# Kernel optimization log

Hardware: AMD Instinct MI355X
Metric: run time of the kernel (lower is better)

## Reference

```python
import jax, jax.numpy as jnp
import numpy as np

RADIUS = 0.4
NSAMPLE = 32


def setup_inputs() -> dict:
    key = jax.random.key(0)
    ks = jax.random.split(key, 6)
    B, N, C = 2, 16384, 64
    xyz = jax.random.normal(ks[0], (B, N, 3), jnp.float32)
    features = jax.random.normal(ks[1], (B, C, N), jnp.float32)

    def w(k, i, o):
        return jax.random.normal(k, (i, o), jnp.float32) * (1.0 / np.sqrt(i))

    W1 = w(ks[2], C + 3, 64)
    W2 = w(ks[3], 64, 64)
    W3 = w(ks[4], 64, 128)
    return {
        "xyz": xyz, "features": features,
        "W1": W1, "b1": jnp.zeros((64,), jnp.float32),
        "W2": W2, "b2": jnp.zeros((64,), jnp.float32),
        "W3": W3, "b3": jnp.zeros((128,), jnp.float32),
        "npoint": 4096,
    }


def ball_query(xyz, new_xyz, radius, nsample):
    """xyz [B,N,3], new_xyz [B,S,3] -> neighbor idx [B,S,nsample] int32.
    Replicates pointnet2 ball_query: first `nsample` points (in index order)
    within `radius` of each centroid; empty slots filled with the first hit
    (0 if no point is in range)."""
    N = xyz.shape[1]
    # squared distances [B,S,N] via ||a||^2 + ||b||^2 - 2 a.b
    d2 = (jnp.sum(new_xyz * new_xyz, -1)[:, :, None]
          + jnp.sum(xyz * xyz, -1)[:, None, :]
          - 2.0 * jnp.einsum('bsc,bnc->bsn', new_xyz, xyz))
    cand = jnp.where(d2 < radius * radius,
                     jnp.arange(N, dtype=jnp.int32), jnp.int32(N))
    neg_topk, _ = jax.lax.top_k(-cand, nsample)  # nsample smallest indices
    idx = -neg_topk
    first = idx[..., :1]
    idx = jnp.where(idx == N, first, idx)  # pad with first valid neighbor
    idx = jnp.where(idx == N, 0, idx)      # no neighbor at all -> 0
    return idx


def reference(xyz, features, W1, b1, W2, b2, W3, b3, npoint):
    B = xyz.shape[0]
    # sample_method=None, keep_first_half=False -> idx = arange(npoint)
    new_xyz = xyz[:, :npoint]                        # [B,S,3]
    idx = ball_query(jax.lax.stop_gradient(xyz),
                     jax.lax.stop_gradient(new_xyz), RADIUS, NSAMPLE)
    # group: gather neighbors, re-center xyz, concat features (use_xyz=True)
    grouped_xyz = jax.vmap(lambda p, i: p[i])(xyz, idx) - new_xyz[:, :, None]  # [B,S,K,3]
    feats_nc = features.transpose(0, 2, 1)           # [B,N,C]
    grouped_f = jax.vmap(lambda f, i: f[i])(feats_nc, idx)  # [B,S,K,C]
    g = jnp.concatenate([grouped_xyz, grouped_f], axis=-1)  # [B,S,K,3+C]
    # shared MLP (1x1 convs + ReLU)
    h = jax.nn.relu(jnp.einsum('bskc,cd->bskd', g, W1) + b1)
    h = jax.nn.relu(jnp.einsum('bskc,cd->bskd', h, W2) + b2)
    h = jax.nn.relu(jnp.einsum('bskc,cd->bskd', h, W3) + b3)
    new_features = jnp.max(h, axis=2).transpose(0, 2, 1)    # [B,128,S]
    samp_idx = jnp.tile(jnp.arange(npoint, dtype=jnp.int32), (B, 1))
    return new_xyz, new_features, samp_idx
```

## Files before the change

kernel.cpp:

```cpp
#include <hip/hip_runtime.h>

#define BB 2
#define NN 16384
#define CC 64
#define SS 4096
#define KK 32
#define R2 0.16f

#define GD   24
#define GC   (GD * GD * GD)
#define CAPC 112
#define CAP  512
#define CAPL (CAP / 64)

typedef __bf16 bf16x8 __attribute__((ext_vector_type(8)));
typedef float  f32x4  __attribute__((ext_vector_type(4)));

#define MFMA(a, b, c) __builtin_amdgcn_mfma_f32_16x16x32_bf16((a), (b), (c), 0, 0, 0)

static __device__ __forceinline__ ushort f2bf(float f) {
    __bf16 h = (__bf16)f;
    return *(ushort*)&h;
}

static __device__ __forceinline__ int cellc(float x) {
    int i = (int)floorf(x * 2.5f + 12.0f);
    return i < 0 ? 0 : (i > GD - 1 ? GD - 1 : i);
}

#define WS_PTS4   0
#define WS_FEAT   524288
#define WS_W1T    4718592
#define WS_W2T    4730880
#define WS_W3T    4739072
#define WS_CNT    4755456
#define WS_LIST   4866048
#define WS_LPTS   17252352

#define T_PTS   (BB * NN)
#define T_W1    (T_PTS + 64 * 96)
#define T_W2    (T_W1 + 64 * 64)
#define T_W3    (T_W2 + 128 * 64)
#define T_NXYZ  (T_W3 + BB * SS * 3)
#define T_SIDX  (T_NXYZ + BB * SS)
#define FEAT_B0 (T_SIDX / 256)
#define NBLK    (FEAT_B0 + BB * (NN / 32))

__global__ __launch_bounds__(256) void prep_kernel(
        const float* __restrict__ xyz, const float* __restrict__ feat,
        const float* __restrict__ W1, const float* __restrict__ W2,
        const float* __restrict__ W3,
        float4* __restrict__ pts4, ushort* __restrict__ feat_nc,
        ushort* __restrict__ W1t, ushort* __restrict__ W2t,
        ushort* __restrict__ W3t,
        float* __restrict__ out_xyz, float* __restrict__ out_sidx,
        uint* __restrict__ counts, int* __restrict__ list,
        float4* __restrict__ lpts) {
    if (blockIdx.x >= FEAT_B0) {
        __shared__ float tile[64][33];
        const int g = blockIdx.x - FEAT_B0;
        const int b = g >> 9, n0 = (g & 511) << 5;
        const int t = threadIdx.x;
        const float* fb = feat + (size_t)b * CC * NN + n0;
        #pragma unroll
        for (int cc = 0; cc < 8; ++cc) {
            const int c = cc * 8 + (t >> 5);
            tile[c][t & 31] = fb[(size_t)c * NN + (t & 31)];
        }
        __syncthreads();
        const int p = t >> 3, c8 = t & 7;
        uint u[4];
        #pragma unroll
        for (int q = 0; q < 4; ++q) {
            u[q] = (uint)f2bf(tile[c8 * 8 + 2 * q][p]) |
                   ((uint)f2bf(tile[c8 * 8 + 2 * q + 1][p]) << 16);
        }
        *(uint4*)(feat_nc + ((size_t)b * NN + n0 + p) * 64 + c8 * 8) =
            make_uint4(u[0], u[1], u[2], u[3]);
        return;
    }
    const int t = blockIdx.x * 256 + threadIdx.x;
    if (t < T_PTS) {
        const float* p = xyz + (size_t)t * 3;
        const float x = p[0], y = p[1], z = p[2];
        const float4 pv = make_float4(x, y, z, x * x + y * y + z * z);
        pts4[t] = pv;
        const int cell = (cellc(z) * GD + cellc(y)) * GD + cellc(x);
        const int b = t >> 14, n = t & (NN - 1);
        const uint rank = atomicAdd(&counts[(size_t)b * GC + cell], 1u);
        if (rank < CAPC) {
            const size_t slot = ((size_t)b * GC + cell) * CAPC + rank;
            list[slot] = n;
            lpts[slot] = pv;
        }
    } else if (t < T_W1) {
        const int i = t - T_PTS;
        const int n = i / 96, k = i - n * 96;
        float v = 0.0f;
        if (k < 64) v = W1[(3 + k) * 64 + n];
        else if (k < 67) v = W1[(k - 64) * 64 + n];
        W1t[n * 96 + k] = f2bf(v);
    } else if (t < T_W2) {
        const int i = t - T_W1;
        const int n = i >> 6, k = i & 63;
        W2t[n * 64 + k] = f2bf(W2[k * 64 + n]);
    } else if (t < T_W3) {
        const int i = t - T_W2;
        const int n = i >> 6, k = i & 63;
        W3t[n * 64 + k] = f2bf(W3[k * 128 + n]);
    } else if (t < T_NXYZ) {
        const int i = t - T_W3;
        const int b = i / (SS * 3), j = i - b * (SS * 3);
        out_xyz[i] = xyz[(size_t)b * NN * 3 + j];
    } else if (t < T_SIDX) {
        const int i = t - T_NXYZ;
        out_sidx[i] = (float)(i & (SS - 1));
    }
}

__global__ __launch_bounds__(256, 2) void fused_kernel(
        const float4* __restrict__ pts4, const ushort* __restrict__ feat_nc,
        const uint* __restrict__ counts, const int* __restrict__ list,
        const float4* __restrict__ lpts,
        const ushort* __restrict__ W1t, const ushort* __restrict__ W2t,
        const ushort* __restrict__ W3t,
        const float* __restrict__ b1, const float* __restrict__ b2,
        const float* __restrict__ b3, float* __restrict__ out_feat) {
    const int w = threadIdx.x >> 6, lane = threadIdx.x & 63;
    const int quad = lane >> 4, mrow = lane & 15;
    const int m = lane & 31, half = lane >> 5;

    __shared__ __align__(16) ushort ldsA[4][32 * 104];
    __shared__ float stage[128][5];
    ushort* gbuf = ldsA[w];
    int* hit = (int*)gbuf;

    const int xcd = blockIdx.x & 7;
    const int slot = blockIdx.x >> 3;
    const int b = xcd >> 2;
    const int s0 = ((xcd & 3) * 256 + slot) * 4;
    const int s = s0 + w;

    const float4* pb = pts4 + (size_t)b * NN;
    const ushort* fbase = feat_nc + (size_t)b * NN * 64;
    const unsigned long long ltmask = (1ull << lane) - 1ull;

    {
        const float4 c = pb[s];
        const int cx = cellc(c.x), cy = cellc(c.y), cz = cellc(c.z);
        const uint* cntb = counts + (size_t)b * GC;
        const int* listb = list + (size_t)b * GC * CAPC;
        const float4* lptsb = lpts + (size_t)b * GC * CAPC;

        int pre[28], A[27];
        pre[0] = 0;
        #pragma unroll
        for (int e = 0; e < 27; ++e) {
            const int z = cz + e / 9 - 1;
            const int y = cy + (e / 3) % 3 - 1;
            const int x = cx + e % 3 - 1;
            const bool ok = ((unsigned)z < GD) && ((unsigned)y < GD) && ((unsigned)x < GD);
            const int ci = (z * GD + y) * GD + x;
            int cn = ok ? (int)cntb[ci] : 0;
            cn = cn < CAPC ? cn : CAPC;
            A[e] = ci * CAPC - pre[e];
            pre[e + 1] = pre[e] + cn;
        }
        const int tot = pre[27];

        int cnt = 0;
        for (int g0 = 0; g0 < tot; g0 += 64) {
            const int g = g0 + lane;
            int adj = A[0];
            #pragma unroll
            for (int k = 1; k < 27; ++k) adj = (g >= pre[k]) ? A[k] : adj;
            const bool act = g < tot;
            const int ga = act ? (g + adj) : 0;
            const float4 p = lptsb[ga];
            const float d = c.w + p.w - 2.0f * (c.x * p.x + c.y * p.y + c.z * p.z);
            const bool h = act && (d < R2);
            const unsigned long long mk = __ballot(h);
            if (h) {
                const int pp = cnt + __popcll(mk & ltmask);
                if (pp < CAP) hit[pp] = listb[ga];
            }
            cnt += (int)__popcll(mk);
        }

        if (cnt > KK) {
            const int stored = cnt < CAP ? cnt : CAP;
            int v[CAPL];
            #pragma unroll
            for (int j = 0; j < CAPL; ++j) {
                const int q = j * 64 + lane;
                const int val = hit[q];
                v[j] = (q < stored) ? val : 0x7fffffff;
            }
            int lo = 0, hi = NN - 1;
            while (lo < hi) {
                const int mid = (lo + hi) >> 1;
                int cle = 0;
                #pragma unroll
                for (int j = 0; j < CAPL; ++j)
                    if (j * 64 < stored)
                        cle += (int)__popcll(__ballot(v[j] <= mid));
                if (cle >= KK) hi = mid; else lo = mid + 1;
            }
            int pos = 0;
            #pragma unroll
            for (int j = 0; j < CAPL; ++j) {
                if (j * 64 < stored) {
                    const bool sel = v[j] <= lo;
                    const unsigned long long mk = __ballot(sel);
                    if (sel) hit[pos + __popcll(mk & ltmask)] = v[j];
                    pos += (int)__popcll(mk);
                }
            }
        } else if (lane < KK) {
            const int vv = (cnt == 0) ? 0 : ((lane < cnt) ? hit[lane] : hit[0]);
            hit[lane] = vv;
        }
    }

    {
        const int sid = hit[m];
        const ushort* src = fbase + (size_t)sid * 64 + half * 32;
        ushort* dst = gbuf + m * 104 + half * 32;
        uint4 rows[4];
        #pragma unroll
        for (int i = 0; i < 4; ++i) rows[i] = *(const uint4*)(src + i * 8);
        const float4 p = pb[sid];
        const float4 cc = pb[s];
        #pragma unroll
        for (int i = 0; i < 4; ++i) *(uint4*)(dst + i * 8) = rows[i];
        if (half == 0) {
            bf16x8 rel = {(__bf16)(p.x - cc.x), (__bf16)(p.y - cc.y),
                          (__bf16)(p.z - cc.z), (__bf16)0.f,
                          (__bf16)0.f, (__bf16)0.f, (__bf16)0.f, (__bf16)0.f};
            *(bf16x8*)(gbuf + m * 104 + 64) = rel;
            *(uint4*)(gbuf + m * 104 + 88) = make_uint4(0, 0, 0, 0);
        } else {
            *(uint4*)(gbuf + m * 104 + 72) = make_uint4(0, 0, 0, 0);
            *(uint4*)(gbuf + m * 104 + 80) = make_uint4(0, 0, 0, 0);
        }
    }

    {
        f32x4 acc[2][4];
        #pragma unroll
        for (int nt = 0; nt < 4; ++nt) {
            const float bv = b1[nt * 16 + mrow];
            acc[0][nt] = (f32x4){bv, bv, bv, bv};
            acc[1][nt] = acc[0][nt];
        }
        #pragma unroll
        for (int ks = 0; ks < 3; ++ks) {
            const bf16x8 a0 = *(const bf16x8*)(gbuf + mrow * 104 + ks * 32 + quad * 8);
            const bf16x8 a1 = *(const bf16x8*)(gbuf + (16 + mrow) * 104 + ks * 32 + quad * 8);
            #pragma unroll
            for (int nt = 0; nt < 4; ++nt) {
                const bf16x8 wf = *(const bf16x8*)(W1t + (nt * 16 + mrow) * 96 + ks * 32 + quad * 8);
                acc[0][nt] = MFMA(a0, wf, acc[0][nt]);
                acc[1][nt] = MFMA(a1, wf, acc[1][nt]);
            }
        }
        #pragma unroll
        for (int mt = 0; mt < 2; ++mt)
            #pragma unroll
            for (int nt = 0; nt < 4; ++nt)
                #pragma unroll
                for (int r = 0; r < 4; ++r)
                    gbuf[(mt * 16 + quad * 4 + r) * 104 + nt * 16 + mrow] =
                        f2bf(fmaxf(acc[mt][nt][r], 0.0f));
    }

    {
        f32x4 acc[2][4];
        #pragma unroll
        for (int nt = 0; nt < 4; ++nt) {
            const float bv = b2[nt * 16 + mrow];
            acc[0][nt] = (f32x4){bv, bv, bv, bv};
            acc[1][nt] = acc[0][nt];
        }
        #pragma unroll
        for (int ks = 0; ks < 2; ++ks) {
            const bf16x8 a0 = *(const bf16x8*)(gbuf + mrow * 104 + ks * 32 + quad * 8);
            const bf16x8 a1 = *(const bf16x8*)(gbuf + (16 + mrow) * 104 + ks * 32 + quad * 8);
            #pragma unroll
            for (int nt = 0; nt < 4; ++nt) {
                const bf16x8 wf = *(const bf16x8*)(W2t + (nt * 16 + mrow) * 64 + ks * 32 + quad * 8);
                acc[0][nt] = MFMA(a0, wf, acc[0][nt]);
                acc[1][nt] = MFMA(a1, wf, acc[1][nt]);
            }
        }
        #pragma unroll
        for (int mt = 0; mt < 2; ++mt)
            #pragma unroll
            for (int nt = 0; nt < 4; ++nt)
                #pragma unroll
                for (int r = 0; r < 4; ++r)
                    gbuf[(mt * 16 + quad * 4 + r) * 104 + nt * 16 + mrow] =
                        f2bf(fmaxf(acc[mt][nt][r], 0.0f));
    }

    #pragma unroll
    for (int nh = 0; nh < 2; ++nh) {
        f32x4 acc[2][4];
        #pragma unroll
        for (int ntl = 0; ntl < 4; ++ntl) {
            const float bv = b3[(nh * 4 + ntl) * 16 + mrow];
            acc[0][ntl] = (f32x4){bv, bv, bv, bv};
            acc[1][ntl] = acc[0][ntl];
        }
        #pragma unroll
        for (int ks = 0; ks < 2; ++ks) {
            const bf16x8 a0 = *(const bf16x8*)(gbuf + mrow * 104 + ks * 32 + quad * 8);
            const bf16x8 a1 = *(const bf16x8*)(gbuf + (16 + mrow) * 104 + ks * 32 + quad * 8);
            #pragma unroll
            for (int ntl = 0; ntl < 4; ++ntl) {
                const bf16x8 wf = *(const bf16x8*)(
                    W3t + ((nh * 4 + ntl) * 16 + mrow) * 64 + ks * 32 + quad * 8);
                acc[0][ntl] = MFMA(a0, wf, acc[0][ntl]);
                acc[1][ntl] = MFMA(a1, wf, acc[1][ntl]);
            }
        }
        #pragma unroll
        for (int ntl = 0; ntl < 4; ++ntl) {
            const f32x4 v0 = acc[0][ntl], v1 = acc[1][ntl];
            float mx = fmaxf(fmaxf(v0[0], v0[1]), fmaxf(v0[2], v0[3]));
            mx = fmaxf(mx, fmaxf(fmaxf(v1[0], v1[1]), fmaxf(v1[2], v1[3])));
            mx = fmaxf(mx, __shfl_xor(mx, 16));
            mx = fmaxf(mx, __shfl_xor(mx, 32));
            mx = fmaxf(mx, 0.0f);
            if (quad == 0) stage[(nh * 4 + ntl) * 16 + mrow][w] = mx;
        }
    }
    __syncthreads();

    {
        const int ch = threadIdx.x & 127;
        const int hf = threadIdx.x >> 7;
        float* dst = out_feat + ((size_t)b * 128 + ch) * SS + s0 + hf * 2;
        *(float2*)dst = make_float2(stage[ch][hf * 2], stage[ch][hf * 2 + 1]);
    }
}

extern "C" void kernel_launch(void* const* d_in, const int* in_sizes, int n_in,
                              void* d_out, int out_size, void* d_ws, size_t ws_size,
                              hipStream_t stream) {
    const float* xyz  = (const float*)d_in[0];
    const float* feat = (const float*)d_in[1];
    const float* W1   = (const float*)d_in[2];
    const float* b1   = (const float*)d_in[3];
    const float* W2   = (const float*)d_in[4];
    const float* b2   = (const float*)d_in[5];
    const float* W3   = (const float*)d_in[6];
    const float* b3   = (const float*)d_in[7];

    float* out      = (float*)d_out;
    float* out_xyz  = out;
    float* out_feat = out + (size_t)BB * SS * 3;
    float* out_sidx = out_feat + (size_t)BB * 128 * SS;

    char* ws = (char*)d_ws;
    float4* pts4    = (float4*)(ws + WS_PTS4);
    ushort* feat_nc = (ushort*)(ws + WS_FEAT);
    ushort* W1t     = (ushort*)(ws + WS_W1T);
    ushort* W2t     = (ushort*)(ws + WS_W2T);
    ushort* W3t     = (ushort*)(ws + WS_W3T);
    uint*   counts  = (uint*)(ws + WS_CNT);
    int*    list    = (int*)(ws + WS_LIST);
    float4* lpts    = (float4*)(ws + WS_LPTS);

    hipMemsetAsync(counts, 0, (size_t)BB * GC * 4, stream);
    prep_kernel<<<NBLK, 256, 0, stream>>>(
        xyz, feat, W1, W2, W3, pts4, feat_nc, W1t, W2t, W3t, out_xyz, out_sidx,
        counts, list, lpts);
    fused_kernel<<<BB * SS / 4, 256, 0, stream>>>(pts4, feat_nc, counts, list,
                                                  lpts, W1t, W2t, W3t,
                                                  b1, b2, b3, out_feat);
}
```

Baseline: 144.6 us.

## Pack point index into lpts, prune unreachable cells, prefetch candidates, reuse LDS

The separate neighbor index list is removed: each binned point stores its index in the w component of its float4, and the squared norm is recomputed on the fly, so one fewer gather is needed per hit. Neighbor cells whose box lies farther than the radius from the centroid are now skipped through a point-to-box distance test, which shrinks the candidate count. The candidate load for the next 64-wide chunk is software-prefetched before the current chunk is processed. The staging array for the output is folded into unused padding of the existing LDS tile to save shared memory. The cost is extra ALU work for the box tests and higher register pressure from the prefetch.

```diff
diff --git a/kernel.cpp b/kernel.cpp
--- a/kernel.cpp
+++ b/kernel.cpp
@@ -34,8 +34,7 @@
 #define WS_W2T    4730880
 #define WS_W3T    4739072
 #define WS_CNT    4755456
-#define WS_LIST   4866048
-#define WS_LPTS   17252352
+#define WS_LPTS   4866048
 
 #define T_PTS   (BB * NN)
 #define T_W1    (T_PTS + 64 * 96)
@@ -54,8 +53,7 @@
         ushort* __restrict__ W1t, ushort* __restrict__ W2t,
         ushort* __restrict__ W3t,
         float* __restrict__ out_xyz, float* __restrict__ out_sidx,
-        uint* __restrict__ counts, int* __restrict__ list,
-        float4* __restrict__ lpts) {
+        uint* __restrict__ counts, float4* __restrict__ lpts) {
     if (blockIdx.x >= FEAT_B0) {
         __shared__ float tile[64][33];
         const int g = blockIdx.x - FEAT_B0;
@@ -83,15 +81,13 @@
     if (t < T_PTS) {
         const float* p = xyz + (size_t)t * 3;
         const float x = p[0], y = p[1], z = p[2];
-        const float4 pv = make_float4(x, y, z, x * x + y * y + z * z);
-        pts4[t] = pv;
+        pts4[t] = make_float4(x, y, z, x * x + y * y + z * z);
         const int cell = (cellc(z) * GD + cellc(y)) * GD + cellc(x);
         const int b = t >> 14, n = t & (NN - 1);
         const uint rank = atomicAdd(&counts[(size_t)b * GC + cell], 1u);
         if (rank < CAPC) {
             const size_t slot = ((size_t)b * GC + cell) * CAPC + rank;
-            list[slot] = n;
-            lpts[slot] = pv;
+            lpts[slot] = make_float4(x, y, z, __int_as_float(n));
         }
     } else if (t < T_W1) {
         const int i = t - T_PTS;
@@ -118,10 +114,14 @@
     }
 }
 
+#define ADJ27(gq, adjv) do { adjv = A[0];                                   \
+    _Pragma("unroll")                                                       \
+    for (int k_ = 1; k_ < 27; ++k_) adjv = ((gq) >= pre[k_]) ? A[k_] : adjv;\
+} while (0)
+
 __global__ __launch_bounds__(256, 2) void fused_kernel(
         const float4* __restrict__ pts4, const ushort* __restrict__ feat_nc,
-        const uint* __restrict__ counts, const int* __restrict__ list,
-        const float4* __restrict__ lpts,
+        const uint* __restrict__ counts, const float4* __restrict__ lpts,
         const ushort* __restrict__ W1t, const ushort* __restrict__ W2t,
         const ushort* __restrict__ W3t,
         const float* __restrict__ b1, const float* __restrict__ b2,
@@ -131,7 +131,6 @@
     const int m = lane & 31, half = lane >> 5;
 
     __shared__ __align__(16) ushort ldsA[4][32 * 104];
-    __shared__ float stage[128][5];
     ushort* gbuf = ldsA[w];
     int* hit = (int*)gbuf;
 
@@ -149,7 +148,6 @@
         const float4 c = pb[s];
         const int cx = cellc(c.x), cy = cellc(c.y), cz = cellc(c.z);
         const uint* cntb = counts + (size_t)b * GC;
-        const int* listb = list + (size_t)b * GC * CAPC;
         const float4* lptsb = lpts + (size_t)b * GC * CAPC;
 
         int pre[28], A[27];
@@ -161,7 +159,17 @@
             const int x = cx + e % 3 - 1;
             const bool ok = ((unsigned)z < GD) && ((unsigned)y < GD) && ((unsigned)x < GD);
             const int ci = (z * GD + y) * GD + x;
-            int cn = ok ? (int)cntb[ci] : 0;
+            const float bx0 = (x <= 0)      ? -1e30f : (x - 12) * 0.4f;
+            const float bx1 = (x >= GD - 1) ?  1e30f : (x - 11) * 0.4f;
+            const float by0 = (y <= 0)      ? -1e30f : (y - 12) * 0.4f;
+            const float by1 = (y >= GD - 1) ?  1e30f : (y - 11) * 0.4f;
+            const float bz0 = (z <= 0)      ? -1e30f : (z - 12) * 0.4f;
+            const float bz1 = (z >= GD - 1) ?  1e30f : (z - 11) * 0.4f;
+            const float dx = fmaxf(fmaxf(bx0 - c.x, c.x - bx1), 0.0f);
+            const float dy = fmaxf(fmaxf(by0 - c.y, c.y - by1), 0.0f);
+            const float dz = fmaxf(fmaxf(bz0 - c.z, c.z - bz1), 0.0f);
+            const bool reach = (dx * dx + dy * dy + dz * dz) < (R2 + 1e-3f);
+            int cn = (ok && reach) ? (int)cntb[ok ? ci : 0] : 0;
             cn = cn < CAPC ? cn : CAPC;
             A[e] = ci * CAPC - pre[e];
             pre[e + 1] = pre[e] + cn;
@@ -169,22 +177,30 @@
         const int tot = pre[27];
 
         int cnt = 0;
+        float4 pc;
+        {
+            const int g = lane;
+            int adj; ADJ27(g, adj);
+            pc = lptsb[(g < tot) ? (g + adj) : 0];
+        }
         for (int g0 = 0; g0 < tot; g0 += 64) {
-            const int g = g0 + lane;
-            int adj = A[0];
-            #pragma unroll
-            for (int k = 1; k < 27; ++k) adj = (g >= pre[k]) ? A[k] : adj;
-            const bool act = g < tot;
-            const int ga = act ? (g + adj) : 0;
-            const float4 p = lptsb[ga];
-            const float d = c.w + p.w - 2.0f * (c.x * p.x + c.y * p.y + c.z * p.z);
+            float4 pn;
+            {
+                const int gn = g0 + 64 + lane;
+                int adjn; ADJ27(gn, adjn);
+                pn = lptsb[(gn < tot) ? (gn + adjn) : 0];
+            }
+            const bool act = (g0 + lane) < tot;
+            const float pw = pc.x * pc.x + pc.y * pc.y + pc.z * pc.z;
+            const float d = c.w + pw - 2.0f * (c.x * pc.x + c.y * pc.y + c.z * pc.z);
             const bool h = act && (d < R2);
             const unsigned long long mk = __ballot(h);
             if (h) {
                 const int pp = cnt + __popcll(mk & ltmask);
-                if (pp < CAP) hit[pp] = listb[ga];
+                if (pp < CAP) hit[pp] = __float_as_int(pc.w);
             }
             cnt += (int)__popcll(mk);
+            pc = pn;
         }
 
         if (cnt > KK) {
@@ -332,7 +348,10 @@
             mx = fmaxf(mx, __shfl_xor(mx, 16));
             mx = fmaxf(mx, __shfl_xor(mx, 32));
             mx = fmaxf(mx, 0.0f);
-            if (quad == 0) stage[(nh * 4 + ntl) * 16 + mrow][w] = mx;
+            if (quad == 0) {
+                const int ch = (nh * 4 + ntl) * 16 + mrow;
+                *(float*)((char*)gbuf + (ch >> 2) * 208 + 192 + (ch & 3) * 4) = mx;
+            }
         }
     }
     __syncthreads();
@@ -340,8 +359,11 @@
     {
         const int ch = threadIdx.x & 127;
         const int hf = threadIdx.x >> 7;
+        const int tb = (ch >> 2) * 208 + 192 + (ch & 3) * 4;
+        const float v0 = *(const float*)((const char*)ldsA[hf * 2] + tb);
+        const float v1 = *(const float*)((const char*)ldsA[hf * 2 + 1] + tb);
         float* dst = out_feat + ((size_t)b * 128 + ch) * SS + s0 + hf * 2;
-        *(float2*)dst = make_float2(stage[ch][hf * 2], stage[ch][hf * 2 + 1]);
+        *(float2*)dst = make_float2(v0, v1);
     }
 }
 
@@ -369,14 +391,13 @@
     ushort* W2t     = (ushort*)(ws + WS_W2T);
     ushort* W3t     = (ushort*)(ws + WS_W3T);
     uint*   counts  = (uint*)(ws + WS_CNT);
-    int*    list    = (int*)(ws + WS_LIST);
     float4* lpts    = (float4*)(ws + WS_LPTS);
 
     hipMemsetAsync(counts, 0, (size_t)BB * GC * 4, stream);
     prep_kernel<<<NBLK, 256, 0, stream>>>(
         xyz, feat, W1, W2, W3, pts4, feat_nc, W1t, W2t, W3t, out_xyz, out_sidx,
-        counts, list, lpts);
-    fused_kernel<<<BB * SS / 4, 256, 0, stream>>>(pts4, feat_nc, counts, list,
-                                                  lpts, W1t, W2t, W3t,
-                                                  b1, b2, b3, out_feat);
+        counts, lpts);
+    fused_kernel<<<BB * SS / 4, 256, 0, stream>>>(pts4, feat_nc, counts, lpts,
+                                                  W1t, W2t, W3t, b1, b2, b3,
+                                                  out_feat);
 }
```

New measurement: 139.9 us. 1.03x faster.

## Process centroids per grid cell, sharing neighbor candidates staged in LDS

Applied to the files above, without the earlier changes.

Prep now builds a per-cell list of centroids and a work list of non-empty centroid cells. The fused kernel becomes a grid-stride loop over those cells: each block stages the 27-cell candidate points (xyz plus index packed in w) into LDS once, then its waves run ball query and the MLP for every centroid in that cell. This replaces repeated global gathers of candidate points per centroid and drops the separate index list. The cost is per-cell load imbalance and extra atomics in prep. It also adds hard caps (1536 candidates, 64 centroids per cell) that could silently truncate dense central neighborhoods.

```diff
diff --git a/kernel.cpp b/kernel.cpp
--- a/kernel.cpp
+++ b/kernel.cpp
@@ -10,8 +10,10 @@
 #define GD   24
 #define GC   (GD * GD * GD)
 #define CAPC 112
+#define CCAP 64
 #define CAP  512
 #define CAPL (CAP / 64)
+#define CANDN 1536
 
 typedef __bf16 bf16x8 __attribute__((ext_vector_type(8)));
 typedef float  f32x4  __attribute__((ext_vector_type(4)));
@@ -34,8 +36,12 @@
 #define WS_W2T    4730880
 #define WS_W3T    4739072
 #define WS_CNT    4755456
-#define WS_LIST   4866048
-#define WS_LPTS   17252352
+#define WS_CCNT   4866048
+#define WS_WLC    4976640
+#define WS_WL     4976656
+#define WS_LPTS   5009424
+#define WS_CSLOT  54554640
+#define MEMSET_B  221200
 
 #define T_PTS   (BB * NN)
 #define T_W1    (T_PTS + 64 * 96)
@@ -54,8 +60,9 @@
         ushort* __restrict__ W1t, ushort* __restrict__ W2t,
         ushort* __restrict__ W3t,
         float* __restrict__ out_xyz, float* __restrict__ out_sidx,
-        uint* __restrict__ counts, int* __restrict__ list,
-        float4* __restrict__ lpts) {
+        uint* __restrict__ counts, float4* __restrict__ lpts,
+        uint* __restrict__ ccnt, int* __restrict__ cslot,
+        uint* __restrict__ wlc, uint* __restrict__ wl) {
     if (blockIdx.x >= FEAT_B0) {
         __shared__ float tile[64][33];
         const int g = blockIdx.x - FEAT_B0;
@@ -83,15 +90,23 @@
     if (t < T_PTS) {
         const float* p = xyz + (size_t)t * 3;
         const float x = p[0], y = p[1], z = p[2];
-        const float4 pv = make_float4(x, y, z, x * x + y * y + z * z);
-        pts4[t] = pv;
+        pts4[t] = make_float4(x, y, z, x * x + y * y + z * z);
         const int cell = (cellc(z) * GD + cellc(y)) * GD + cellc(x);
         const int b = t >> 14, n = t & (NN - 1);
         const uint rank = atomicAdd(&counts[(size_t)b * GC + cell], 1u);
         if (rank < CAPC) {
             const size_t slot = ((size_t)b * GC + cell) * CAPC + rank;
-            list[slot] = n;
-            lpts[slot] = pv;
+            lpts[slot] = make_float4(x, y, z, __int_as_float(n));
+        }
+        if (n < SS) {
+            const uint rk = atomicAdd(&ccnt[(size_t)b * GC + cell], 1u);
+            if (rk < CCAP) {
+                cslot[((size_t)b * GC + cell) * CCAP + rk] = n;
+                if (rk == 0) {
+                    const uint wi = atomicAdd(wlc, 1u);
+                    wl[wi] = ((uint)b << 16) | (uint)cell;
+                }
+            }
         }
     } else if (t < T_W1) {
         const int i = t - T_PTS;
@@ -120,8 +135,9 @@
 
 __global__ __launch_bounds__(256, 2) void fused_kernel(
         const float4* __restrict__ pts4, const ushort* __restrict__ feat_nc,
-        const uint* __restrict__ counts, const int* __restrict__ list,
-        const float4* __restrict__ lpts,
+        const uint* __restrict__ counts, const float4* __restrict__ lpts,
+        const uint* __restrict__ ccnt, const int* __restrict__ cslot,
+        const uint* __restrict__ wlc, const uint* __restrict__ wl,
         const ushort* __restrict__ W1t, const ushort* __restrict__ W2t,
         const ushort* __restrict__ W3t,
         const float* __restrict__ b1, const float* __restrict__ b2,
@@ -130,218 +146,226 @@
     const int quad = lane >> 4, mrow = lane & 15;
     const int m = lane & 31, half = lane >> 5;
 
+    __shared__ __align__(16) float4 cand[CANDN];
     __shared__ __align__(16) ushort ldsA[4][32 * 104];
-    __shared__ float stage[128][5];
     ushort* gbuf = ldsA[w];
     int* hit = (int*)gbuf;
-
-    const int xcd = blockIdx.x & 7;
-    const int slot = blockIdx.x >> 3;
-    const int b = xcd >> 2;
-    const int s0 = ((xcd & 3) * 256 + slot) * 4;
-    const int s = s0 + w;
-
-    const float4* pb = pts4 + (size_t)b * NN;
-    const ushort* fbase = feat_nc + (size_t)b * NN * 64;
     const unsigned long long ltmask = (1ull << lane) - 1ull;
 
-    {
-        const float4 c = pb[s];
-        const int cx = cellc(c.x), cy = cellc(c.y), cz = cellc(c.z);
+    const uint nwl = *wlc;
+    for (uint wi = blockIdx.x; wi < nwl; wi += gridDim.x) {
+        __syncthreads();
+        const uint wle = wl[wi];
+        const int b = (int)(wle >> 16), cell = (int)(wle & 0xffffu);
+        const int czc = cell / (GD * GD);
+        const int rem = cell - czc * GD * GD;
+        const int cyc = rem / GD, cxc = rem % GD;
+
+        const float4* pb = pts4 + (size_t)b * NN;
+        const ushort* fbase = feat_nc + (size_t)b * NN * 64;
         const uint* cntb = counts + (size_t)b * GC;
-        const int* listb = list + (size_t)b * GC * CAPC;
         const float4* lptsb = lpts + (size_t)b * GC * CAPC;
 
-        int pre[28], A[27];
+        int pre[28], baseE[27];
         pre[0] = 0;
         #pragma unroll
         for (int e = 0; e < 27; ++e) {
-            const int z = cz + e / 9 - 1;
-            const int y = cy + (e / 3) % 3 - 1;
-            const int x = cx + e % 3 - 1;
+            const int z = czc + e / 9 - 1;
+            const int y = cyc + (e / 3) % 3 - 1;
+            const int x = cxc + e % 3 - 1;
             const bool ok = ((unsigned)z < GD) && ((unsigned)y < GD) && ((unsigned)x < GD);
             const int ci = (z * GD + y) * GD + x;
-            int cn = ok ? (int)cntb[ci] : 0;
+            int cn = ok ? (int)cntb[ok ? ci : 0] : 0;
             cn = cn < CAPC ? cn : CAPC;
-            A[e] = ci * CAPC - pre[e];
+            if (cn > CANDN - pre[e]) cn = CANDN - pre[e];
+            baseE[e] = ci * CAPC;
             pre[e + 1] = pre[e] + cn;
         }
         const int tot = pre[27];
 
-        int cnt = 0;
-        for (int g0 = 0; g0 < tot; g0 += 64) {
-            const int g = g0 + lane;
-            int adj = A[0];
+        for (int e = w; e < 27; e += 4) {
+            const int cn = pre[e + 1] - pre[e];
+            if (lane < cn) cand[pre[e] + lane] = lptsb[baseE[e] + lane];
+            if (cn > 64 && lane + 64 < cn)
+                cand[pre[e] + 64 + lane] = lptsb[baseE[e] + 64 + lane];
+        }
+        __syncthreads();
+
+        const uint ncr = ccnt[(size_t)b * GC + cell];
+        const int nc = (int)(ncr < CCAP ? ncr : CCAP);
+        for (int i = w; i < nc; i += 4) {
+            const int s = cslot[((size_t)b * GC + cell) * CCAP + i];
+            const float4 c = pb[s];
+
+            int cnt = 0;
+            for (int g0 = 0; g0 < tot; g0 += 64) {
+                const int g = g0 + lane;
+                const float4 pc = cand[g < tot ? g : 0];
+                const bool act = g < tot;
+                const float pw = pc.x * pc.x + pc.y * pc.y + pc.z * pc.z;
+                const float d = c.w + pw - 2.0f * (c.x * pc.x + c.y * pc.y + c.z * pc.z);
+                const bool h = act && (d < R2);
+                const unsigned long long mk = __ballot(h);
+                if (h) {
+                    const int pp = cnt + __popcll(mk & ltmask);
+                    if (pp < CAP) hit[pp] = __float_as_int(pc.w);
+                }
+                cnt += (int)__popcll(mk);
+            }
+
+            if (cnt > KK) {
+                const int stored = cnt < CAP ? cnt : CAP;
+                int v[CAPL];
+                #pragma unroll
+                for (int j = 0; j < CAPL; ++j) {
+                    if (j * 64 < stored) {
+                        const int q = j * 64 + lane;
+                        v[j] = (q < stored) ? hit[q] : 0x7fffffff;
+                    } else {
+                        v[j] = 0x7fffffff;
+                    }
+                }
+                int lo = 0, hi = NN - 1;
+                while (lo < hi) {
+                    const int mid = (lo + hi) >> 1;
+                    int cle = 0;
+                    #pragma unroll
+                    for (int j = 0; j < CAPL; ++j)
+                        if (j * 64 < stored)
+                            cle += (int)__popcll(__ballot(v[j] <= mid));
+                    if (cle >= KK) hi = mid; else lo = mid + 1;
+                }
+                int pos = 0;
+                #pragma unroll
+                for (int j = 0; j < CAPL; ++j) {
+                    if (j * 64 < stored) {
+                        const bool sel = v[j] <= lo;
+                        const unsigned long long mk = __ballot(sel);
+                        if (sel) hit[pos + __popcll(mk & ltmask)] = v[j];
+                        pos += (int)__popcll(mk);
+                    }
+                }
+            } else if (lane < KK) {
+                const int vv = (cnt == 0) ? 0 : ((lane < cnt) ? hit[lane] : hit[0]);
+                hit[lane] = vv;
+            }
+
+            {
+                const int sid = hit[m];
+                const ushort* src = fbase + (size_t)sid * 64 + half * 32;
+                ushort* dst = gbuf + m * 104 + half * 32;
+                uint4 rows[4];
+                #pragma unroll
+                for (int i2 = 0; i2 < 4; ++i2) rows[i2] = *(const uint4*)(src + i2 * 8);
+                const float4 p = pb[sid];
+                #pragma unroll
+                for (int i2 = 0; i2 < 4; ++i2) *(uint4*)(dst + i2 * 8) = rows[i2];
+                if (half == 0) {
+                    bf16x8 rel = {(__bf16)(p.x - c.x), (__bf16)(p.y - c.y),
+                                  (__bf16)(p.z - c.z), (__bf16)0.f,
+                                  (__bf16)0.f, (__bf16)0.f, (__bf16)0.f, (__bf16)0.f};
+                    *(bf16x8*)(gbuf + m * 104 + 64) = rel;
+                    *(uint4*)(gbuf + m * 104 + 88) = make_uint4(0, 0, 0, 0);
+                } else {
+                    *(uint4*)(gbuf + m * 104 + 72) = make_uint4(0, 0, 0, 0);
+                    *(uint4*)(gbuf + m * 104 + 80) = make_uint4(0, 0, 0, 0);
+                }
+            }
+
+            {
+                f32x4 acc[2][4];
+                #pragma unroll
+                for (int nt = 0; nt < 4; ++nt) {
+                    const float bv = b1[nt * 16 + mrow];
+                    acc[0][nt] = (f32x4){bv, bv, bv, bv};
+                    acc[1][nt] = acc[0][nt];
+                }
+                #pragma unroll
+                for (int ks = 0; ks < 3; ++ks) {
+                    const bf16x8 a0 = *(const bf16x8*)(gbuf + mrow * 104 + ks * 32 + quad * 8);
+                    const bf16x8 a1 = *(const bf16x8*)(gbuf + (16 + mrow) * 104 + ks * 32 + quad * 8);
+                    #pragma unroll
+                    for (int nt = 0; nt < 4; ++nt) {
+                        const bf16x8 wf = *(const bf16x8*)(W1t + (nt * 16 + mrow) * 96 + ks * 32 + quad * 8);
+                        acc[0][nt] = MFMA(a0, wf, acc[0][nt]);
+                        acc[1][nt] = MFMA(a1, wf, acc[1][nt]);
+                    }
+                }
+                #pragma unroll
+                for (int mt = 0; mt < 2; ++mt)
+                    #pragma unroll
+                    for (int nt = 0; nt < 4; ++nt)
+                        #pragma unroll
+                        for (int r = 0; r < 4; ++r)
+                            gbuf[(mt * 16 + quad * 4 + r) * 104 + nt * 16 + mrow] =
+                                f2bf(fmaxf(acc[mt][nt][r], 0.0f));
+            }
+
+            {
+                f32x4 acc[2][4];
+                #pragma unroll
+                for (int nt = 0; nt < 4; ++nt) {
+                    const float bv = b2[nt * 16 + mrow];
+                    acc[0][nt] = (f32x4){bv, bv, bv, bv};
+                    acc[1][nt] = acc[0][nt];
+                }
+                #pragma unroll
+                for (int ks = 0; ks < 2; ++ks) {
+                    const bf16x8 a0 = *(const bf16x8*)(gbuf + mrow * 104 + ks * 32 + quad * 8);
+                    const bf16x8 a1 = *(const bf16x8*)(gbuf + (16 + mrow) * 104 + ks * 32 + quad * 8);
+                    #pragma unroll
+                    for (int nt = 0; nt < 4; ++nt) {
+                        const bf16x8 wf = *(const bf16x8*)(W2t + (nt * 16 + mrow) * 64 + ks * 32 + quad * 8);
+                        acc[0][nt] = MFMA(a0, wf, acc[0][nt]);
+                        acc[1][nt] = MFMA(a1, wf, acc[1][nt]);
+                    }
+                }
+                #pragma unroll
+                for (int mt = 0; mt < 2; ++mt)
+                    #pragma unroll
+                    for (int nt = 0; nt < 4; ++nt)
+                        #pragma unroll
+                        for (int r = 0; r < 4; ++r)
+                            gbuf[(mt * 16 + quad * 4 + r) * 104 + nt * 16 + mrow] =
+                                f2bf(fmaxf(acc[mt][nt][r], 0.0f));
+            }
+
             #pragma unroll
-            for (int k = 1; k < 27; ++k) adj = (g >= pre[k]) ? A[k] : adj;
-            const bool act = g < tot;
-            const int ga = act ? (g + adj) : 0;
-            const float4 p = lptsb[ga];
-            const float d = c.w + p.w - 2.0f * (c.x * p.x + c.y * p.y + c.z * p.z);
-            const bool h = act && (d < R2);
-            const unsigned long long mk = __ballot(h);
-            if (h) {
-                const int pp = cnt + __popcll(mk & ltmask);
-                if (pp < CAP) hit[pp] = listb[ga];
-            }
-            cnt += (int)__popcll(mk);
-        }
-
-        if (cnt > KK) {
-            const int stored = cnt < CAP ? cnt : CAP;
-            int v[CAPL];
-            #pragma unroll
-            for (int j = 0; j < CAPL; ++j) {
-                const int q = j * 64 + lane;
-                const int val = hit[q];
-                v[j] = (q < stored) ? val : 0x7fffffff;
-            }
-            int lo = 0, hi = NN - 1;
-            while (lo < hi) {
-                const int mid = (lo + hi) >> 1;
-                int cle = 0;
-                #pragma unroll
-                for (int j = 0; j < CAPL; ++j)
-                    if (j * 64 < stored)
-                        cle += (int)__popcll(__ballot(v[j] <= mid));
-                if (cle >= KK) hi = mid; else lo = mid + 1;
-            }
-            int pos = 0;
-            #pragma unroll
-            for (int j = 0; j < CAPL; ++j) {
-                if (j * 64 < stored) {
-                    const bool sel = v[j] <= lo;
-                    const unsigned long long mk = __ballot(sel);
-                    if (sel) hit[pos + __popcll(mk & ltmask)] = v[j];
-                    pos += (int)__popcll(mk);
-                }
-            }
-        } else if (lane < KK) {
-            const int vv = (cnt == 0) ? 0 : ((lane < cnt) ? hit[lane] : hit[0]);
-            hit[lane] = vv;
-        }
-    }
-
-    {
-        const int sid = hit[m];
-        const ushort* src = fbase + (size_t)sid * 64 + half * 32;
-        ushort* dst = gbuf + m * 104 + half * 32;
-        uint4 rows[4];
-        #pragma unroll
-        for (int i = 0; i < 4; ++i) rows[i] = *(const uint4*)(src + i * 8);
-        const float4 p = pb[sid];
-        const float4 cc = pb[s];
-        #pragma unroll
-        for (int i = 0; i < 4; ++i) *(uint4*)(dst + i * 8) = rows[i];
-        if (half == 0) {
-            bf16x8 rel = {(__bf16)(p.x - cc.x), (__bf16)(p.y - cc.y),
-                          (__bf16)(p.z - cc.z), (__bf16)0.f,
-                          (__bf16)0.f, (__bf16)0.f, (__bf16)0.f, (__bf16)0.f};
-            *(bf16x8*)(gbuf + m * 104 + 64) = rel;
-            *(uint4*)(gbuf + m * 104 + 88) = make_uint4(0, 0, 0, 0);
-        } else {
-            *(uint4*)(gbuf + m * 104 + 72) = make_uint4(0, 0, 0, 0);
-            *(uint4*)(gbuf + m * 104 + 80) = make_uint4(0, 0, 0, 0);
-        }
-    }
-
-    {
-        f32x4 acc[2][4];
-        #pragma unroll
-        for (int nt = 0; nt < 4; ++nt) {
-            const float bv = b1[nt * 16 + mrow];
-            acc[0][nt] = (f32x4){bv, bv, bv, bv};
-            acc[1][nt] = acc[0][nt];
-        }
-        #pragma unroll
-        for (int ks = 0; ks < 3; ++ks) {
-            const bf16x8 a0 = *(const bf16x8*)(gbuf + mrow * 104 + ks * 32 + quad * 8);
-            const bf16x8 a1 = *(const bf16x8*)(gbuf + (16 + mrow) * 104 + ks * 32 + quad * 8);
-            #pragma unroll
-            for (int nt = 0; nt < 4; ++nt) {
-                const bf16x8 wf = *(const bf16x8*)(W1t + (nt * 16 + mrow) * 96 + ks * 32 + quad * 8);
-                acc[0][nt] = MFMA(a0, wf, acc[0][nt]);
-                acc[1][nt] = MFMA(a1, wf, acc[1][nt]);
-            }
-        }
-        #pragma unroll
-        for (int mt = 0; mt < 2; ++mt)
-            #pragma unroll
-            for (int nt = 0; nt < 4; ++nt)
-                #pragma unroll
-                for (int r = 0; r < 4; ++r)
-                    gbuf[(mt * 16 + quad * 4 + r) * 104 + nt * 16 + mrow] =
-                        f2bf(fmaxf(acc[mt][nt][r], 0.0f));
-    }
-
-    {
-        f32x4 acc[2][4];
-        #pragma unroll
-        for (int nt = 0; nt < 4; ++nt) {
-            const float bv = b2[nt * 16 + mrow];
-            acc[0][nt] = (f32x4){bv, bv, bv, bv};
-            acc[1][nt] = acc[0][nt];
-        }
-        #pragma unroll
-        for (int ks = 0; ks < 2; ++ks) {
-            const bf16x8 a0 = *(const bf16x8*)(gbuf + mrow * 104 + ks * 32 + quad * 8);
-            const bf16x8 a1 = *(const bf16x8*)(gbuf + (16 + mrow) * 104 + ks * 32 + quad * 8);
-            #pragma unroll
-            for (int nt = 0; nt < 4; ++nt) {
-                const bf16x8 wf = *(const bf16x8*)(W2t + (nt * 16 + mrow) * 64 + ks * 32 + quad * 8);
-                acc[0][nt] = MFMA(a0, wf, acc[0][nt]);
-                acc[1][nt] = MFMA(a1, wf, acc[1][nt]);
-            }
-        }
-        #pragma unroll
-        for (int mt = 0; mt < 2; ++mt)
-            #pragma unroll
-            for (int nt = 0; nt < 4; ++nt)
-                #pragma unroll
-                for (int r = 0; r < 4; ++r)
-                    gbuf[(mt * 16 + quad * 4 + r) * 104 + nt * 16 + mrow] =
-                        f2bf(fmaxf(acc[mt][nt][r], 0.0f));
-    }
-
-    #pragma unroll
-    for (int nh = 0; nh < 2; ++nh) {
-        f32x4 acc[2][4];
-        #pragma unroll
-        for (int ntl = 0; ntl < 4; ++ntl) {
-            const float bv = b3[(nh * 4 + ntl) * 16 + mrow];
-            acc[0][ntl] = (f32x4){bv, bv, bv, bv};
-            acc[1][ntl] = acc[0][ntl];
-        }
-        #pragma unroll
-        for (int ks = 0; ks < 2; ++ks) {
-            const bf16x8 a0 = *(const bf16x8*)(gbuf + mrow * 104 + ks * 32 + quad * 8);
-            const bf16x8 a1 = *(const bf16x8*)(gbuf + (16 + mrow) * 104 + ks * 32 + quad * 8);
-            #pragma unroll
-            for (int ntl = 0; ntl < 4; ++ntl) {
-                const bf16x8 wf = *(const bf16x8*)(
-                    W3t + ((nh * 4 + ntl) * 16 + mrow) * 64 + ks * 32 + quad * 8);
-                acc[0][ntl] = MFMA(a0, wf, acc[0][ntl]);
-                acc[1][ntl] = MFMA(a1, wf, acc[1][ntl]);
-            }
-        }
-        #pragma unroll
-        for (int ntl = 0; ntl < 4; ++ntl) {
-            const f32x4 v0 = acc[0][ntl], v1 = acc[1][ntl];
-            float mx = fmaxf(fmaxf(v0[0], v0[1]), fmaxf(v0[2], v0[3]));
-            mx = fmaxf(mx, fmaxf(fmaxf(v1[0], v1[1]), fmaxf(v1[2], v1[3])));
-            mx = fmaxf(mx, __shfl_xor(mx, 16));
-            mx = fmaxf(mx, __shfl_xor(mx, 32));
-            mx = fmaxf(mx, 0.0f);
-            if (quad == 0) stage[(nh * 4 + ntl) * 16 + mrow][w] = mx;
-        }
-    }
-    __syncthreads();
-
-    {
-        const int ch = threadIdx.x & 127;
-        const int hf = threadIdx.x >> 7;
-        float* dst = out_feat + ((size_t)b * 128 + ch) * SS + s0 + hf * 2;
-        *(float2*)dst = make_float2(stage[ch][hf * 2], stage[ch][hf * 2 + 1]);
+            for (int nh = 0; nh < 2; ++nh) {
+                f32x4 acc[2][4];
+                #pragma unroll
+                for (int ntl = 0; ntl < 4; ++ntl) {
+                    const float bv = b3[(nh * 4 + ntl) * 16 + mrow];
+                    acc[0][ntl] = (f32x4){bv, bv, bv, bv};
+                    acc[1][ntl] = acc[0][ntl];
+                }
+                #pragma unroll
+                for (int ks = 0; ks < 2; ++ks) {
+                    const bf16x8 a0 = *(const bf16x8*)(gbuf + mrow * 104 + ks * 32 + quad * 8);
+                    const bf16x8 a1 = *(const bf16x8*)(gbuf + (16 + mrow) * 104 + ks * 32 + quad * 8);
+                    #pragma unroll
+                    for (int ntl = 0; ntl < 4; ++ntl) {
+                        const bf16x8 wf = *(const bf16x8*)(
+                            W3t + ((nh * 4 + ntl) * 16 + mrow) * 64 + ks * 32 + quad * 8);
+                        acc[0][ntl] = MFMA(a0, wf, acc[0][ntl]);
+                        acc[1][ntl] = MFMA(a1, wf, acc[1][ntl]);
+                    }
+                }
+                #pragma unroll
+                for (int ntl = 0; ntl < 4; ++ntl) {
+                    const f32x4 v0 = acc[0][ntl], v1 = acc[1][ntl];
+                    float mx = fmaxf(fmaxf(v0[0], v0[1]), fmaxf(v0[2], v0[3]));
+                    mx = fmaxf(mx, fmaxf(fmaxf(v1[0], v1[1]), fmaxf(v1[2], v1[3])));
+                    mx = fmaxf(mx, __shfl_xor(mx, 16));
+                    mx = fmaxf(mx, __shfl_xor(mx, 32));
+                    mx = fmaxf(mx, 0.0f);
+                    if (quad == 0) {
+                        const int ch = (nh * 4 + ntl) * 16 + mrow;
+                        out_feat[((size_t)b * 128 + ch) * SS + s] = mx;
+                    }
+                }
+            }
+        }
     }
 }
 
@@ -369,14 +393,17 @@
     ushort* W2t     = (ushort*)(ws + WS_W2T);
     ushort* W3t     = (ushort*)(ws + WS_W3T);
     uint*   counts  = (uint*)(ws + WS_CNT);
-    int*    list    = (int*)(ws + WS_LIST);
+    uint*   ccnt    = (uint*)(ws + WS_CCNT);
+    uint*   wlc     = (uint*)(ws + WS_WLC);
+    uint*   wl      = (uint*)(ws + WS_WL);
     float4* lpts    = (float4*)(ws + WS_LPTS);
-
-    hipMemsetAsync(counts, 0, (size_t)BB * GC * 4, stream);
+    int*    cslot   = (int*)(ws + WS_CSLOT);
+
+    hipMemsetAsync(counts, 0, MEMSET_B, stream);
     prep_kernel<<<NBLK, 256, 0, stream>>>(
         xyz, feat, W1, W2, W3, pts4, feat_nc, W1t, W2t, W3t, out_xyz, out_sidx,
-        counts, list, lpts);
-    fused_kernel<<<BB * SS / 4, 256, 0, stream>>>(pts4, feat_nc, counts, list,
-                                                  lpts, W1t, W2t, W3t,
-                                                  b1, b2, b3, out_feat);
+        counts, lpts, ccnt, cslot, wlc, wl);
+    fused_kernel<<<2048, 256, 0, stream>>>(pts4, feat_nc, counts, lpts,
+                                           ccnt, cslot, wlc, wl,
+                                           W1t, W2t, W3t, b1, b2, b3, out_feat);
 }
```

Result: slower. 287.9 us (+99.1%).
